# Kernel optimization log

Measured on AMD Instinct MI355X. Metric: run time of the kernel, lower is better.

Reference implementation:

```python
import jax, jax.numpy as jnp
import numpy as np

H = 8  # n_heads from init_kwargs
EPS = 1e-5


def _ln(x, g, b):
    m = jnp.mean(x, axis=-1, keepdims=True)
    v = jnp.mean((x - m) ** 2, axis=-1, keepdims=True)
    return (x - m) * jax.lax.rsqrt(v + EPS) * g + b


def setup_inputs() -> dict:
    key = jax.random.key(0)
    B, d_m, n, L, p_d = 1, 256, 128, 1024, 128
    ks = jax.random.split(key, 12)
    s = 0.02
    return {
        "msa": jax.random.normal(ks[0], (B, d_m, n, L), jnp.float32),
        "pairs": jax.random.normal(ks[1], (B, n, n, p_d), jnp.float32),
        "ln_m_g": jnp.ones((d_m,), jnp.float32),
        "ln_m_b": jnp.zeros((d_m,), jnp.float32),
        "ln_p_g": jnp.ones((p_d,), jnp.float32),
        "ln_p_b": jnp.zeros((p_d,), jnp.float32),
        "Wq": jax.random.normal(ks[2], (d_m, d_m), jnp.float32) * s,
        "Wk": jax.random.normal(ks[3], (d_m, d_m), jnp.float32) * s,
        "Wv": jax.random.normal(ks[4], (d_m, d_m), jnp.float32) * s,
        "Wg": jax.random.normal(ks[5], (d_m, d_m), jnp.float32) * s,
        "bg": jnp.zeros((d_m,), jnp.float32),
        "Wb": jax.random.normal(ks[6], (p_d, H), jnp.float32) * s,
        "Wo": jax.random.normal(ks[7], (d_m, d_m), jnp.float32) * s,
        "bo": jnp.zeros((d_m,), jnp.float32),
    }


def reference(msa, pairs, ln_m_g, ln_m_b, ln_p_g, ln_p_b,
              Wq, Wk, Wv, Wg, bg, Wb, Wo, bo):
    B, d_m, n, L = msa.shape
    dh = d_m // H
    sqrt_c = jnp.sqrt(jnp.asarray(dh, msa.dtype))

    x = _ln(jnp.transpose(msa, (0, 3, 2, 1)), ln_m_g, ln_m_b)      # [B,L,n,d_m]
    p = _ln(pairs, ln_p_g, ln_p_b)                                   # [B,n,n,p_d]

    # pair bias: (B,n,n,H) -> (B,1,H,n_q,n_k)
    bias = jnp.transpose(jnp.einsum('bijc,ch->bijh', p, Wb), (0, 3, 1, 2))[:, None]

    def heads(y):  # [B,L,n,d_m] -> [B,L,H,n,dh]
        return jnp.transpose(y.reshape(B, L, n, H, dh), (0, 1, 3, 2, 4))

    q = heads(x @ Wq)
    k = heads(x @ Wk)
    v = heads(x @ Wv)
    g = jax.nn.sigmoid(heads(x @ Wg + bg))

    scores = jnp.einsum('blhnd,blhmd->blhnm', q, k) / sqrt_c + bias  # [B,L,H,n,n]
    w = jax.nn.softmax(scores, axis=-1)
    attn = g * jnp.einsum('blhnm,blhmd->blhnd', w, v)                # [B,L,H,n,dh]

    attn = jnp.transpose(attn, (0, 1, 3, 2, 4)).reshape(B, L, n, d_m)
    out = attn @ Wo + bo                                             # [B,L,n,d_m]
    return jnp.transpose(out, (0, 3, 2, 1))                          # [B,d_m,n,L]
```

## Files before the change

kernel.cpp:

```cpp
#include <hip/hip_runtime.h>

__device__ __forceinline__ float bf1(unsigned short s){ return __uint_as_float((unsigned)s << 16); }
__device__ __forceinline__ unsigned short f2bf(float f){
  unsigned u = __float_as_uint(f);
  u += 0x7fffu + ((u >> 16) & 1u);
  return (unsigned short)(u >> 16);
}
__device__ __forceinline__ unsigned cvt_pk_bf16(float a, float b){
  unsigned r;
  asm("v_cvt_pk_bf16_f32 %0, %1, %2" : "=v"(r) : "v"(a), "v"(b));
  return r;
}

typedef __attribute__((ext_vector_type(8))) short short8;
typedef __attribute__((ext_vector_type(4))) float f32x4;

__device__ __forceinline__ f32x4 mfma16(short8 a, short8 b, f32x4 c){
  return __builtin_amdgcn_mfma_f32_16x16x32_bf16(a, b, c, 0, 0, 0);
}

#define GLOAD_LDS16(g, l) \
  __builtin_amdgcn_global_load_lds((const __attribute__((address_space(1))) unsigned int*)(g), \
                                   (__attribute__((address_space(3))) unsigned int*)(l), 16, 0, 0)

__global__ __launch_bounds__(256) void ln_msa_kernel(
    const float* __restrict__ msa, const float* __restrict__ gam,
    const float* __restrict__ bet, unsigned short* __restrict__ x16)
{
  __shared__ float tile[256*33];
  __shared__ float ps[8*32], pq[8*32];
  __shared__ float mean_s[32], rstd_s[32];
  const int t = threadIdx.x;
  const int l0 = blockIdx.x * 32;
  const int n  = blockIdx.y;
  {
    const int lt = t & 31, ct = t >> 5;
    for (int r = 0; r < 32; ++r) {
      int c = r*8 + ct;
      tile[c*33 + lt] = msa[(size_t)c*131072 + (size_t)n*1024 + l0 + lt];
    }
  }
  __syncthreads();
  {
    const int lt = t & 31, cp = t >> 5;
    float s1 = 0.f, s2 = 0.f;
    for (int cc = 0; cc < 32; ++cc) {
      int c = cp*32 + ((cc + cp*4) & 31);
      float v = tile[c*33 + lt];
      s1 += v; s2 += v*v;
    }
    ps[cp*32 + lt] = s1; pq[cp*32 + lt] = s2;
  }
  __syncthreads();
  if (t < 32) {
    float s1 = 0.f, s2 = 0.f;
    for (int cp = 0; cp < 8; ++cp){ s1 += ps[cp*32+t]; s2 += pq[cp*32+t]; }
    float m = s1 * (1.f/256.f);
    float v = s2 * (1.f/256.f) - m*m;
    mean_s[t] = m;
    rstd_s[t] = rsqrtf(v + 1e-5f);
  }
  __syncthreads();
  {
    const float g = gam[t], b = bet[t];
    for (int l = 0; l < 32; ++l) {
      float v = (tile[t*33 + l] - mean_s[l]) * rstd_s[l] * g + b;
      x16[((size_t)(l0+l)*128 + n)*256 + t] = f2bf(v);
    }
  }
}

__global__ __launch_bounds__(64) void pair_bias_kernel(
    const float* __restrict__ pairs, const float* __restrict__ gam,
    const float* __restrict__ bet, const float* __restrict__ Wb,
    float* __restrict__ biasb)
{
  const int j = blockIdx.x, i = blockIdx.y;
  const int t = threadIdx.x;
  const float* row = pairs + ((size_t)i*128 + j)*128;
  float v0 = row[t], v1 = row[t+64];
  float s = v0 + v1;
  #pragma unroll
  for (int o = 1; o < 64; o <<= 1) s += __shfl_xor(s, o, 64);
  float m = s * (1.f/128.f);
  float d0 = v0 - m, d1 = v1 - m;
  float q = d0*d0 + d1*d1;
  #pragma unroll
  for (int o = 1; o < 64; o <<= 1) q += __shfl_xor(q, o, 64);
  float rstd = rsqrtf(q * (1.f/128.f) + 1e-5f);
  float n0 = d0 * rstd * gam[t]    + bet[t];
  float n1 = d1 * rstd * gam[t+64] + bet[t+64];
  #pragma unroll
  for (int h = 0; h < 8; ++h) {
    float p = n0 * Wb[t*8 + h] + n1 * Wb[(t+64)*8 + h];
    #pragma unroll
    for (int o = 1; o < 64; o <<= 1) p += __shfl_xor(p, o, 64);
    if (t == h) biasb[((size_t)h*128 + i)*128 + j] = p;
  }
}

__global__ __launch_bounds__(256) void wprep_kernel(
    const float* __restrict__ Wq, const float* __restrict__ Wk,
    const float* __restrict__ Wv, const float* __restrict__ Wg,
    const float* __restrict__ Wo,
    unsigned short* __restrict__ Wt, unsigned short* __restrict__ WoT)
{
  const int n = blockIdx.x, k = threadIdx.x;
  if (n < 1024) {
    const int mat = n >> 8, nl = n & 255;
    const float* W = (mat==0) ? Wq : (mat==1) ? Wk : (mat==2) ? Wv : Wg;
    float v = W[(size_t)k*256 + nl];
    if (mat == 0) v *= 0.17677669529663689f;
    Wt[(size_t)n*256 + k] = f2bf(v);
  } else {
    const int c = n - 1024;
    WoT[(size_t)c*256 + k] = f2bf(Wo[(size_t)k*256 + c]);
  }
}

#define QP 40
#define VP 136
__global__ __launch_bounds__(512) void fused_qkvg_attn(
    const unsigned short* __restrict__ X, const unsigned short* __restrict__ Wt,
    const float* __restrict__ bg, const float* __restrict__ biasb,
    unsigned short* __restrict__ attn2)
{
  __shared__ __align__(16) unsigned short lds[69888];
  unsigned short* Xs  = lds;
  unsigned short* qs  = lds + 32768;
  unsigned short* ks  = lds + 37888;
  unsigned short* gs  = lds + 43008;
  unsigned short* vs  = lds + 48128;
  unsigned short* pbuf= lds + 52480;

  const int t = threadIdx.x, l = blockIdx.x;
  const int w = t>>6, fr = t&15, quad = (t>>4)&3;
  const int mat = w>>1, dh = (w&1)*16;
  const int d0 = dh + quad*4;
  unsigned short* pw = pbuf + w*2176;
  const int rbase = w*16;
  const f32x4 zero4 = {0.f,0.f,0.f,0.f};

  #pragma unroll
  for (int s = 0; s < 8; ++s) {
    int cid = s*512 + t;
    int k0b = cid>>10, r = (cid>>3)&127, pch = cid&7;
    int c = pch ^ (r&7);
    const unsigned short* g = X + ((size_t)l*128 + r)*256 + k0b*64 + c*8;
    GLOAD_LDS16(g, Xs + (cid & ~63)*8);
  }

  const unsigned short* wptr = Wt + ((size_t)(mat*256 + dh + fr))*256 + quad*8;
  short8 wreg[8];
  #pragma unroll
  for (int i = 0; i < 8; ++i)
    wreg[i] = *(const short8*)(wptr + (i>>1)*64 + (i&1)*32);

  for (int h = 0; h < 8; ++h) {
    __syncthreads();

    f32x4 acc[8] = {};
    #pragma unroll
    for (int k0 = 0; k0 < 4; ++k0) {
      #pragma unroll
      for (int kt = 0; kt < 2; ++kt) {
        const int ck = kt*4 + quad;
        const short8 bf = wreg[k0*2 + kt];
        #pragma unroll
        for (int mt = 0; mt < 8; ++mt) {
          const int r = mt*16 + fr;
          short8 af = *(const short8*)(Xs + k0*8192 + r*64 + (ck^(r&7))*8);
          acc[mt] = mfma16(bf, af, acc[mt]);
        }
      }
    }

    if (h < 7) {
      const unsigned short* wn = wptr + (size_t)(h+1)*8192;
      #pragma unroll
      for (int i = 0; i < 8; ++i)
        wreg[i] = *(const short8*)(wn + (i>>1)*64 + (i&1)*32);
    }

    if (mat == 2) {
      #pragma unroll
      for (int mt = 0; mt < 8; ++mt) {
        const int m = mt*16 + fr;
        #pragma unroll
        for (int reg = 0; reg < 4; ++reg) {
          const int d = d0 + reg;
          vs[d*VP + (((m>>3)^(d&7))<<3) + (m&7)] = f2bf(acc[mt][reg]);
        }
      }
    } else {
      unsigned short* buf = (mat==0) ? qs : (mat==1) ? ks : gs;
      float4 b4;
      if (mat == 3) b4 = *(const float4*)(bg + h*32 + d0);
      #pragma unroll
      for (int mt = 0; mt < 8; ++mt) {
        const int m = mt*16 + fr;
        float v0 = acc[mt][0], v1 = acc[mt][1], v2 = acc[mt][2], v3 = acc[mt][3];
        if (mat == 3) {
          v0 = 1.f/(1.f + __expf(-(v0 + b4.x)));
          v1 = 1.f/(1.f + __expf(-(v1 + b4.y)));
          v2 = 1.f/(1.f + __expf(-(v2 + b4.z)));
          v3 = 1.f/(1.f + __expf(-(v3 + b4.w)));
        }
        uint2 pk;
        pk.x = cvt_pk_bf16(v0, v1);
        pk.y = cvt_pk_bf16(v2, v3);
        *(uint2*)(buf + m*QP + d0) = pk;
      }
    }
    __syncthreads();

    short8 aq = *(const short8*)(qs + (rbase+fr)*QP + quad*8);
    f32x4 S[8];
    #pragma unroll
    for (int nt=0;nt<8;++nt) {
      short8 bk = *(const short8*)(ks + (nt*16+fr)*QP + quad*8);
      S[nt] = mfma16(aq, bk, zero4);
    }
    const float* bb = biasb + ((size_t)h*128 + rbase + quad*4)*128 + fr;
    #pragma unroll
    for (int nt=0;nt<8;++nt)
      #pragma unroll
      for (int reg=0;reg<4;++reg)
        S[nt][reg] += bb[(size_t)reg*128 + nt*16];
    float mx[4] = {-1e30f,-1e30f,-1e30f,-1e30f};
    #pragma unroll
    for (int nt=0;nt<8;++nt)
      #pragma unroll
      for (int reg=0;reg<4;++reg) mx[reg] = fmaxf(mx[reg], S[nt][reg]);
    #pragma unroll
    for (int reg=0;reg<4;++reg) {
      mx[reg] = fmaxf(mx[reg], __shfl_xor(mx[reg], 1, 64));
      mx[reg] = fmaxf(mx[reg], __shfl_xor(mx[reg], 2, 64));
      mx[reg] = fmaxf(mx[reg], __shfl_xor(mx[reg], 4, 64));
      mx[reg] = fmaxf(mx[reg], __shfl_xor(mx[reg], 8, 64));
    }
    float sum[4] = {0.f,0.f,0.f,0.f};
    #pragma unroll
    for (int nt=0;nt<8;++nt)
      #pragma unroll
      for (int reg=0;reg<4;++reg) {
        float e = __expf(S[nt][reg]-mx[reg]);
        S[nt][reg] = e; sum[reg] += e;
      }
    #pragma unroll
    for (int reg=0;reg<4;++reg) {
      sum[reg] += __shfl_xor(sum[reg], 1, 64);
      sum[reg] += __shfl_xor(sum[reg], 2, 64);
      sum[reg] += __shfl_xor(sum[reg], 4, 64);
      sum[reg] += __shfl_xor(sum[reg], 8, 64);
    }
    float inv[4];
    #pragma unroll
    for (int reg=0;reg<4;++reg) inv[reg] = 1.f/sum[reg];
    #pragma unroll
    for (int nt=0;nt<8;++nt)
      #pragma unroll
      for (int reg=0;reg<4;++reg)
        pw[(quad*4+reg)*136 + nt*16 + fr] = f2bf(S[nt][reg]*inv[reg]);
    asm volatile("s_waitcnt lgkmcnt(0)" ::: "memory");
    f32x4 o[2] = {zero4, zero4};
    #pragma unroll
    for (int kt=0;kt<4;++kt) {
      short8 ap = *(const short8*)(pw + fr*136 + kt*32 + quad*8);
      #pragma unroll
      for (int n2=0;n2<2;++n2) {
        const int d = n2*16 + fr;
        const int ph = (kt*4+quad) ^ (d&7);
        short8 bv = *(const short8*)(vs + d*VP + ph*8);
        o[n2] = mfma16(ap, bv, o[n2]);
      }
    }
    #pragma unroll
    for (int n2=0;n2<2;++n2)
      #pragma unroll
      for (int reg=0;reg<4;++reg) {
        const int row = rbase + quad*4 + reg, col = n2*16 + fr;
        const float gv = bf1(gs[row*QP + col]);
        attn2[((size_t)row*1024 + l)*256 + h*32 + col] = f2bf(o[n2][reg]*gv);
      }
    __syncthreads();
  }
}

__global__ __launch_bounds__(256) void outproj_mfma(
    const unsigned short* __restrict__ attn2, const unsigned short* __restrict__ WoT,
    const float* __restrict__ bo, float* __restrict__ out)
{
  __shared__ __align__(16) unsigned short As[128*64], Bs[128*64];
  const int t = threadIdx.x;
  const int c0 = blockIdx.x*128;
  const int l0 = blockIdx.y*128;
  const int n  = blockIdx.z;
  const int w = t>>6, lane = t&63, fr = lane&15, quad = lane>>4;
  const int wm = (w>>1)*64, wn = (w&1)*64;
  f32x4 acc[4][4] = {};
  for (int k0 = 0; k0 < 256; k0 += 64) {
    if (k0) __syncthreads();
    #pragma unroll
    for (int pss = 0; pss < 4; ++pss) {
      int s = pss*256 + t;
      int row = s >> 3, pch = s & 7;
      int c = pch ^ (row & 7);
      const unsigned short* ga = WoT   + (size_t)(c0+row)*256 + k0 + c*8;
      const unsigned short* gb = attn2 + ((size_t)n*1024 + l0 + row)*256 + k0 + c*8;
      GLOAD_LDS16(ga, As + (s & ~63)*8);
      GLOAD_LDS16(gb, Bs + (s & ~63)*8);
    }
    __syncthreads();
    #pragma unroll
    for (int kt = 0; kt < 2; ++kt) {
      short8 af[4], bfr[4];
      #pragma unroll
      for (int mt=0;mt<4;++mt){ int r = wm+mt*16+fr; int ch = (kt*4+quad)^(r&7);
        af[mt] = *(const short8*)(As + r*64 + ch*8); }
      #pragma unroll
      for (int nt=0;nt<4;++nt){ int r = wn+nt*16+fr; int ch = (kt*4+quad)^(r&7);
        bfr[nt] = *(const short8*)(Bs + r*64 + ch*8); }
      #pragma unroll
      for (int mt=0;mt<4;++mt)
        #pragma unroll
        for (int nt=0;nt<4;++nt)
          acc[mt][nt] = mfma16(af[mt], bfr[nt], acc[mt][nt]);
    }
  }
  #pragma unroll
  for (int mt=0;mt<4;++mt) {
    #pragma unroll
    for (int reg=0;reg<4;++reg) {
      const int c = c0 + wm + mt*16 + quad*4 + reg;
      const float bv = bo[c];
      #pragma unroll
      for (int nt=0;nt<4;++nt) {
        const int l = l0 + wn + nt*16 + fr;
        out[(size_t)c*131072 + (size_t)n*1024 + l] = acc[mt][nt][reg] + bv;
      }
    }
  }
}

extern "C" void kernel_launch(void* const* d_in, const int* in_sizes, int n_in,
                              void* d_out, int out_size, void* d_ws, size_t ws_size,
                              hipStream_t stream) {
  const float* msa    = (const float*)d_in[0];
  const float* pairs  = (const float*)d_in[1];
  const float* ln_m_g = (const float*)d_in[2];
  const float* ln_m_b = (const float*)d_in[3];
  const float* ln_p_g = (const float*)d_in[4];
  const float* ln_p_b = (const float*)d_in[5];
  const float* Wq     = (const float*)d_in[6];
  const float* Wk     = (const float*)d_in[7];
  const float* Wv     = (const float*)d_in[8];
  const float* Wg     = (const float*)d_in[9];
  const float* bg     = (const float*)d_in[10];
  const float* Wb     = (const float*)d_in[11];
  const float* Wo     = (const float*)d_in[12];
  const float* bo     = (const float*)d_in[13];
  float* out = (float*)d_out;

  char* ws = (char*)d_ws;
  unsigned short* attn2= (unsigned short*)(ws);
  unsigned short* x16  = (unsigned short*)(ws + (size_t)268435456);
  float*          biasb= (float*)         (ws + (size_t)335544320);
  unsigned short* Wt   = (unsigned short*)(ws + (size_t)336068608);
  unsigned short* WoT  = (unsigned short*)(ws + (size_t)336592896);

  hipLaunchKernelGGL(ln_msa_kernel, dim3(32,128), dim3(256), 0, stream,
                     msa, ln_m_g, ln_m_b, x16);
  hipLaunchKernelGGL(pair_bias_kernel, dim3(128,128), dim3(64), 0, stream,
                     pairs, ln_p_g, ln_p_b, Wb, biasb);
  hipLaunchKernelGGL(wprep_kernel, dim3(1280), dim3(256), 0, stream,
                     Wq, Wk, Wv, Wg, Wo, Wt, WoT);
  hipLaunchKernelGGL(fused_qkvg_attn, dim3(1024), dim3(512), 0, stream,
                     x16, Wt, bg, biasb, attn2);
  hipLaunchKernelGGL(outproj_mfma, dim3(2,8,128), dim3(256), 0, stream,
                     attn2, WoT, bo, out);
}
```

Baseline: 591.6 us.

## Software-pipeline next head's QKVG projection with current head's attention

Restructures the per-head loop so the projection GEMM for head h+1 is issued between the QK^T MFMAs and the softmax of head h. V is double-buffered in LDS, and gate values are read into registers before the barrier so the next head's epilogue can overwrite q/k/g. This lets MFMA projection work overlap with softmax and bias loads and removes one barrier per head. In exchange it raises register pressure and adds an occupancy hint (launch_bounds 512,2) plus an extra projection computed at the wrap-around.

```diff
diff --git a/kernel.cpp b/kernel.cpp
--- a/kernel.cpp
+++ b/kernel.cpp
@@ -119,24 +119,79 @@
 }
 
 #define QP 40
-#define VP 136
-__global__ __launch_bounds__(512) void fused_qkvg_attn(
+__device__ __forceinline__ void gemm_head(
+    const unsigned short* Xs, const short8* wreg, int fr, int quad, f32x4* acc)
+{
+  #pragma unroll
+  for (int k0 = 0; k0 < 4; ++k0) {
+    #pragma unroll
+    for (int kt = 0; kt < 2; ++kt) {
+      const int ck = kt*4 + quad;
+      const short8 bf = wreg[k0*2 + kt];
+      #pragma unroll
+      for (int mt = 0; mt < 8; ++mt) {
+        const int r = mt*16 + fr;
+        short8 af = *(const short8*)(Xs + k0*8192 + r*64 + ((ck^(r&7)))*8);
+        acc[mt] = mfma16(bf, af, acc[mt]);
+      }
+    }
+  }
+}
+
+__device__ __forceinline__ void epilogue_head(
+    const f32x4* acc, int mat, int fr, int quad, int dh, int hh,
+    unsigned short* qs, unsigned short* ks, unsigned short* gs, unsigned short* vnxt,
+    const float* __restrict__ bg)
+{
+  const int d0 = dh + quad*4;
+  if (mat == 2) {
+    #pragma unroll
+    for (int mt = 0; mt < 8; ++mt) {
+      const int m = mt*16 + fr;
+      #pragma unroll
+      for (int reg = 0; reg < 4; ++reg) {
+        const int d = d0 + reg;
+        vnxt[d*128 + (((m>>3)^(d&7))<<3) + (m&7)] = f2bf(acc[mt][reg]);
+      }
+    }
+  } else {
+    unsigned short* buf = (mat==0) ? qs : (mat==1) ? ks : gs;
+    float4 b4 = {0.f,0.f,0.f,0.f};
+    if (mat == 3) b4 = *(const float4*)(bg + hh*32 + d0);
+    #pragma unroll
+    for (int mt = 0; mt < 8; ++mt) {
+      const int m = mt*16 + fr;
+      float v0 = acc[mt][0], v1 = acc[mt][1], v2 = acc[mt][2], v3 = acc[mt][3];
+      if (mat == 3) {
+        v0 = 1.f/(1.f + __expf(-(v0 + b4.x)));
+        v1 = 1.f/(1.f + __expf(-(v1 + b4.y)));
+        v2 = 1.f/(1.f + __expf(-(v2 + b4.z)));
+        v3 = 1.f/(1.f + __expf(-(v3 + b4.w)));
+      }
+      uint2 pk;
+      pk.x = cvt_pk_bf16(v0, v1);
+      pk.y = cvt_pk_bf16(v2, v3);
+      *(uint2*)(buf + m*QP + d0) = pk;
+    }
+  }
+}
+
+__global__ __launch_bounds__(512, 2) void fused_qkvg_attn(
     const unsigned short* __restrict__ X, const unsigned short* __restrict__ Wt,
     const float* __restrict__ bg, const float* __restrict__ biasb,
     unsigned short* __restrict__ attn2)
 {
-  __shared__ __align__(16) unsigned short lds[69888];
+  __shared__ __align__(16) unsigned short lds[73728];
   unsigned short* Xs  = lds;
   unsigned short* qs  = lds + 32768;
   unsigned short* ks  = lds + 37888;
   unsigned short* gs  = lds + 43008;
-  unsigned short* vs  = lds + 48128;
-  unsigned short* pbuf= lds + 52480;
+  unsigned short* vsb = lds + 48128;
+  unsigned short* pbuf= lds + 56320;
 
   const int t = threadIdx.x, l = blockIdx.x;
   const int w = t>>6, fr = t&15, quad = (t>>4)&3;
   const int mat = w>>1, dh = (w&1)*16;
-  const int d0 = dh + quad*4;
   unsigned short* pw = pbuf + w*2176;
   const int rbase = w*16;
   const f32x4 zero4 = {0.f,0.f,0.f,0.f};
@@ -156,63 +211,21 @@
   for (int i = 0; i < 8; ++i)
     wreg[i] = *(const short8*)(wptr + (i>>1)*64 + (i&1)*32);
 
+  __syncthreads();
+
+  {
+    f32x4 acc[8] = {};
+    gemm_head(Xs, wreg, fr, quad, acc);
+    #pragma unroll
+    for (int i = 0; i < 8; ++i)
+      wreg[i] = *(const short8*)(wptr + 8192 + (i>>1)*64 + (i&1)*32);
+    epilogue_head(acc, mat, fr, quad, dh, 0, qs, ks, gs, vsb, bg);
+  }
+  __syncthreads();
+
   for (int h = 0; h < 8; ++h) {
-    __syncthreads();
-
-    f32x4 acc[8] = {};
-    #pragma unroll
-    for (int k0 = 0; k0 < 4; ++k0) {
-      #pragma unroll
-      for (int kt = 0; kt < 2; ++kt) {
-        const int ck = kt*4 + quad;
-        const short8 bf = wreg[k0*2 + kt];
-        #pragma unroll
-        for (int mt = 0; mt < 8; ++mt) {
-          const int r = mt*16 + fr;
-          short8 af = *(const short8*)(Xs + k0*8192 + r*64 + (ck^(r&7))*8);
-          acc[mt] = mfma16(bf, af, acc[mt]);
-        }
-      }
-    }
-
-    if (h < 7) {
-      const unsigned short* wn = wptr + (size_t)(h+1)*8192;
-      #pragma unroll
-      for (int i = 0; i < 8; ++i)
-        wreg[i] = *(const short8*)(wn + (i>>1)*64 + (i&1)*32);
-    }
-
-    if (mat == 2) {
-      #pragma unroll
-      for (int mt = 0; mt < 8; ++mt) {
-        const int m = mt*16 + fr;
-        #pragma unroll
-        for (int reg = 0; reg < 4; ++reg) {
-          const int d = d0 + reg;
-          vs[d*VP + (((m>>3)^(d&7))<<3) + (m&7)] = f2bf(acc[mt][reg]);
-        }
-      }
-    } else {
-      unsigned short* buf = (mat==0) ? qs : (mat==1) ? ks : gs;
-      float4 b4;
-      if (mat == 3) b4 = *(const float4*)(bg + h*32 + d0);
-      #pragma unroll
-      for (int mt = 0; mt < 8; ++mt) {
-        const int m = mt*16 + fr;
-        float v0 = acc[mt][0], v1 = acc[mt][1], v2 = acc[mt][2], v3 = acc[mt][3];
-        if (mat == 3) {
-          v0 = 1.f/(1.f + __expf(-(v0 + b4.x)));
-          v1 = 1.f/(1.f + __expf(-(v1 + b4.y)));
-          v2 = 1.f/(1.f + __expf(-(v2 + b4.z)));
-          v3 = 1.f/(1.f + __expf(-(v3 + b4.w)));
-        }
-        uint2 pk;
-        pk.x = cvt_pk_bf16(v0, v1);
-        pk.y = cvt_pk_bf16(v2, v3);
-        *(uint2*)(buf + m*QP + d0) = pk;
-      }
-    }
-    __syncthreads();
+    unsigned short* vcur = vsb + (h&1)*4096;
+    unsigned short* vnxt = vsb + ((h+1)&1)*4096;
 
     short8 aq = *(const short8*)(qs + (rbase+fr)*QP + quad*8);
     f32x4 S[8];
@@ -220,6 +233,14 @@
     for (int nt=0;nt<8;++nt) {
       short8 bk = *(const short8*)(ks + (nt*16+fr)*QP + quad*8);
       S[nt] = mfma16(aq, bk, zero4);
+    }
+    f32x4 acc[8] = {};
+    gemm_head(Xs, wreg, fr, quad, acc);
+    {
+      const unsigned short* wp = wptr + (size_t)((h+2)&7)*8192;
+      #pragma unroll
+      for (int i = 0; i < 8; ++i)
+        wreg[i] = *(const short8*)(wp + (i>>1)*64 + (i&1)*32);
     }
     const float* bb = biasb + ((size_t)h*128 + rbase + quad*4)*128 + fr;
     #pragma unroll
@@ -257,12 +278,21 @@
     float inv[4];
     #pragma unroll
     for (int reg=0;reg<4;++reg) inv[reg] = 1.f/sum[reg];
+    float gv[2][4];
+    #pragma unroll
+    for (int n2=0;n2<2;++n2)
+      #pragma unroll
+      for (int reg=0;reg<4;++reg)
+        gv[n2][reg] = bf1(gs[(rbase + quad*4 + reg)*QP + n2*16 + fr]);
     #pragma unroll
     for (int nt=0;nt<8;++nt)
       #pragma unroll
       for (int reg=0;reg<4;++reg)
         pw[(quad*4+reg)*136 + nt*16 + fr] = f2bf(S[nt][reg]*inv[reg]);
-    asm volatile("s_waitcnt lgkmcnt(0)" ::: "memory");
+
+    __syncthreads();
+
+    epilogue_head(acc, mat, fr, quad, dh, (h+1)&7, qs, ks, gs, vnxt, bg);
     f32x4 o[2] = {zero4, zero4};
     #pragma unroll
     for (int kt=0;kt<4;++kt) {
@@ -271,7 +301,7 @@
       for (int n2=0;n2<2;++n2) {
         const int d = n2*16 + fr;
         const int ph = (kt*4+quad) ^ (d&7);
-        short8 bv = *(const short8*)(vs + d*VP + ph*8);
+        short8 bv = *(const short8*)(vcur + d*128 + ph*8);
         o[n2] = mfma16(ap, bv, o[n2]);
       }
     }
@@ -280,9 +310,9 @@
       #pragma unroll
       for (int reg=0;reg<4;++reg) {
         const int row = rbase + quad*4 + reg, col = n2*16 + fr;
-        const float gv = bf1(gs[row*QP + col]);
-        attn2[((size_t)row*1024 + l)*256 + h*32 + col] = f2bf(o[n2][reg]*gv);
-      }
+        attn2[((size_t)row*1024 + l)*256 + h*32 + col] = f2bf(o[n2][reg]*gv[n2][reg]);
+      }
+
     __syncthreads();
   }
 }
```

Result: slower. 736.3 us (+24.4%).
